# Kernel tuning notes

Hardware: AMD Instinct MI355X
Metric: run time of the kernel (lower is better)

## Reference

```python
import jax, jax.numpy as jnp
import numpy as np

E = 32          # num_experts
K = 4           # num_experts_per_tok
H = 1024        # hidden_size
I = 768         # moe_intermediate_size
ROUTED_SCALING_FACTOR = 1.0


def setup_inputs() -> dict:
    key = jax.random.key(0)
    k0, k1, k2, k3, k4, k5 = jax.random.split(key, 6)
    return {
        "hidden_states": jax.random.normal(k0, (1, 2048, H), jnp.float32),
        "gate_w": jax.random.normal(k1, (E, H), jnp.float32) * 0.02,
        "w1": jax.random.normal(k2, (E, H, I), jnp.float32) * 0.02,   # gate proj per expert
        "w3": jax.random.normal(k3, (E, H, I), jnp.float32) * 0.02,   # up proj per expert
        "w2": jax.random.normal(k4, (E, I, H), jnp.float32) * 0.02,   # down proj per expert
        "e_bias": jax.random.normal(k5, (E,), jnp.float32) * 0.02,    # e_score_correction_bias
    }


def reference(hidden_states, gate_w, w1, w3, w2, e_bias):
    orig_shape = hidden_states.shape
    x = hidden_states.reshape(-1, orig_shape[-1])            # [T, H]
    T = x.shape[0]

    # ----- router gate (ReplicatedLinear, no bias) -----
    router_logits = x @ gate_w.T                             # [T, E]

    # ----- grouped top-k with num_expert_group=1, topk_group=1 == plain top-k
    # scoring_func='sigmoid'; correction bias only affects expert *selection*,
    # the routing weights are the uncorrected sigmoid scores.
    scores = jax.nn.sigmoid(router_logits.astype(jnp.float32))          # [T, E]
    _, topk_ids = jax.lax.top_k(scores + e_bias[None, :], K)            # [T, K]
    topk_w = jnp.take_along_axis(scores, topk_ids, axis=1)              # [T, K]
    # renormalize (norm_topk_prob=True)
    topk_w = topk_w / jnp.sum(topk_w, axis=1, keepdims=True)

    # dense combine weights [T, E] (zero for unselected experts)
    combine = jnp.zeros((T, E), jnp.float32).at[jnp.arange(T)[:, None], topk_ids].add(topk_w)

    # ----- experts: SwiGLU per expert, combine weighted -----
    g = jnp.einsum("th,ehi->tei", x, w1)                     # [T, E, I]
    u = jnp.einsum("th,ehi->tei", x, w3)                     # [T, E, I]
    a = jax.nn.silu(g) * u * combine[:, :, None].astype(x.dtype)
    out = jnp.einsum("tei,eih->th", a, w2)                   # [T, H]

    out = out * ROUTED_SCALING_FACTOR
    return out.reshape(orig_shape)
```

## Files before the change

### kernel.cpp

```cpp
#include <hip/hip_runtime.h>
#include <cstdint>

#define TOK 2048
#define HD  1024
#define ID  768
#define NE  32
#define BM  320
#define NPOS (TOK * 4)

typedef unsigned short u16t;
typedef unsigned int   u32t;
typedef __bf16 bf16x8 __attribute__((ext_vector_type(8)));
typedef float  f32x4  __attribute__((ext_vector_type(4)));
typedef u16t   u16x8  __attribute__((ext_vector_type(8)));
typedef u16t   u16x4  __attribute__((ext_vector_type(4)));
typedef float  fvec4  __attribute__((ext_vector_type(4)));

__device__ __forceinline__ u16t f2b(float f) {
  u32t u = __float_as_uint(f);
  u32t r = u + 0x7fffu + ((u >> 16) & 1u);
  return (u16t)(r >> 16);
}

typedef __attribute__((address_space(3))) unsigned int       lds_uint;
typedef const __attribute__((address_space(1))) unsigned int glob_uint;
__device__ __forceinline__ void gload16(const void* g, void* l) {
  __builtin_amdgcn_global_load_lds((glob_uint*)g, (lds_uint*)l, 16, 0, 0);
}

#define BARN(N) do { \
    asm volatile("s_waitcnt vmcnt(" #N ") lgkmcnt(0)" ::: "memory"); \
    __builtin_amdgcn_s_barrier(); \
    __builtin_amdgcn_sched_barrier(0); \
  } while (0)

__global__ void k_router(const float* __restrict__ x, const float* __restrict__ gw,
                         const float* __restrict__ eb,
                         int* __restrict__ topk_ids, float* __restrict__ topk_w,
                         int* __restrict__ counts) {
  int lane = threadIdx.x & 63;
  int t = blockIdx.x * 4 + (threadIdx.x >> 6);
  const float* xt = x + (size_t)t * HD;
  fvec4 xr[4];
#pragma unroll
  for (int i = 0; i < 4; ++i) xr[i] = *(const fvec4*)(xt + lane * 4 + i * 256);
  float myscore = 0.f;
  for (int e = 0; e < NE; ++e) {
    const float* ge = gw + (size_t)e * HD + lane * 4;
    float s = 0.f;
#pragma unroll
    for (int i = 0; i < 4; ++i) {
      fvec4 g = *(const fvec4*)(ge + i * 256);
      s = fmaf(xr[i][0], g[0], s); s = fmaf(xr[i][1], g[1], s);
      s = fmaf(xr[i][2], g[2], s); s = fmaf(xr[i][3], g[3], s);
    }
#pragma unroll
    for (int off = 32; off; off >>= 1) s += __shfl_xor(s, off);
    if (lane == e) myscore = s;
  }
  float sig = 1.f / (1.f + expf(-myscore));
  float biased = (lane < NE) ? (sig + eb[lane]) : -3.0e38f;
  float wsum = 0.f;
  int ids[4]; float wsv[4];
#pragma unroll
  for (int k = 0; k < 4; ++k) {
    float v = biased; int idx = lane;
#pragma unroll
    for (int off = 32; off; off >>= 1) {
      float ov = __shfl_xor(v, off);
      int   oi = __shfl_xor(idx, off);
      if (ov > v || (ov == v && oi < idx)) { v = ov; idx = oi; }
    }
    ids[k] = idx;
    float sc = __shfl(sig, idx);
    wsv[k] = sc; wsum += sc;
    if (lane == idx) biased = -3.0e38f;
  }
  float inv = 1.f / wsum;
#pragma unroll
  for (int k = 0; k < 4; ++k) {
    if (lane == k) {
      topk_ids[t * 4 + k] = ids[k];
      topk_w[t * 4 + k]  = wsv[k] * inv;
      atomicAdd(&counts[ids[k]], 1);
    }
  }
}

__global__ void k_bucket(const int* __restrict__ topk_ids, const float* __restrict__ topk_w,
                         const int* __restrict__ counts, int* __restrict__ offsets,
                         int* __restrict__ pairTok, float* __restrict__ pairW,
                         int* __restrict__ invp) {
  __shared__ int soff[NE + 1];
  __shared__ int scur[NE];
  int tid = threadIdx.x;
  if (tid == 0) {
    int acc = 0;
    for (int e = 0; e < NE; ++e) { soff[e] = acc; acc += counts[e]; }
    soff[NE] = acc;
  }
  if (tid < NE) scur[tid] = 0;
  __syncthreads();
  if (tid <= NE) offsets[tid] = soff[tid];
  for (int p = tid; p < NPOS; p += 256) {
    int e = topk_ids[p];
    int pos = soff[e] + atomicAdd(&scur[e], 1);
    pairTok[pos] = p;
    pairW[pos]   = topk_w[p];
    invp[p]      = pos;
  }
}

__global__ void k_permute(const float* __restrict__ x, const int* __restrict__ pairTok,
                          u16t* __restrict__ Xp) {
  const int c = blockIdx.x;
  const int t = threadIdx.x;
  const int r = t & 15;
  const int tok = pairTok[c * 16 + r] >> 2;
  const float* xrow = x + (size_t)tok * HD;
  u16t* outp = Xp + (size_t)c * 16384;
#pragma unroll
  for (int i = 0; i < 8; ++i) {
    int G = t + i * 256;
    int s = G >> 6, g = (G >> 4) & 3;
    const float* src = xrow + s * 32 + g * 8;
    fvec4 a = *(const fvec4*)src, b = *(const fvec4*)(src + 4);
    u16x8 o = { f2b(a[0]), f2b(a[1]), f2b(a[2]), f2b(a[3]),
                f2b(b[0]), f2b(b[1]), f2b(b[2]), f2b(b[3]) };
    *(u16x8*)&outp[(size_t)G * 8] = o;
  }
}

__launch_bounds__(256, 3)
__global__ void k_gemm1(const u16t* __restrict__ Xp, const float* __restrict__ w1,
                        const float* __restrict__ w3,
                        const int* __restrict__ counts, const int* __restrict__ offsets,
                        const float* __restrict__ pairW,
                        u16t* __restrict__ A) {
  const int e = blockIdx.y;
  const int colbase = blockIdx.x * 32;
  const int count = counts[e];
  const int base  = offsets[e];
  const int tid = threadIdx.x, lane = tid & 63, wv = tid >> 6;
  const int l15 = lane & 15, kcl = lane >> 4;

  __shared__ __align__(16) u16t Xs[2][20 * 512];
  __shared__ __align__(16) u16t Ws[2][2][1024];
  __shared__ float pw[BM];

  const int mat_s = tid >> 7;
  const int v = tid & 127;
  const int wcolL = v & 31;
  const int kcs = v >> 5;
  const float* wp = (mat_s ? w3 : w1) + (size_t)e * HD * ID
                    + (size_t)(kcs * 8) * ID + colbase + wcolL;

#define G1_STAGEX(P, SMIN) do { \
    _Pragma("unroll") for (int q = 0; q < 5; ++q) \
      gload16((const char*)Xp + xsrc[q] + (u32t)(SMIN) * 1024u, &Xs[P][(wv * 5 + q) * 512]); \
  } while (0)
#define G1_WLOAD(WD, KB) do { \
    _Pragma("unroll") for (int j = 0; j < 8; ++j) \
      WD[j] = wp[(size_t)((KB) + j) * ID]; \
  } while (0)
#define G1_WSTORE(P, WD) do { \
    u16x8 pk = { f2b(WD[0]), f2b(WD[1]), f2b(WD[2]), f2b(WD[3]), \
                 f2b(WD[4]), f2b(WD[5]), f2b(WD[6]), f2b(WD[7]) }; \
    *(u16x8*)&Ws[P][mat_s][kcs * 256 + wcolL * 8] = pk; \
  } while (0)
#define G1_MFMA(P) do { \
    bf16x8 af[5]; \
    _Pragma("unroll") for (int rf = 0; rf < 5; ++rf) \
      af[rf] = *(const bf16x8*)&Xs[P][(wv * 5 + rf) * 512 + kcl * 128 + l15 * 8]; \
    _Pragma("unroll") for (int m = 0; m < 2; ++m) \
      _Pragma("unroll") for (int cf = 0; cf < 2; ++cf) { \
        bf16x8 b = *(const bf16x8*)&Ws[P][m][kcl * 256 + (cf * 16 + l15) * 8]; \
        _Pragma("unroll") for (int rf = 0; rf < 5; ++rf) \
          acc[rf][cf][m] = __builtin_amdgcn_mfma_f32_16x16x32_bf16(af[rf], b, acc[rf][cf][m], 0, 0, 0); \
      } \
  } while (0)

  for (int r0 = 0; r0 < count; r0 += BM) {
    __syncthreads();
    {
      int i = r0 + tid;
      pw[tid] = (i < count) ? pairW[base + i] : 0.f;
      if (tid < BM - 256) {
        int i2 = r0 + 256 + tid;
        pw[256 + tid] = (i2 < count) ? pairW[base + i2] : 0.f;
      }
    }
    u32t xsrc[5];
#pragma unroll
    for (int q = 0; q < 5; ++q) {
      int pos = base + r0 + wv * 80 + q * 16 + l15;
      pos = pos < NPOS ? pos : NPOS - 1;
      xsrc[q] = (u32t)(pos >> 4) * 32768u + (u32t)kcl * 256u + (u32t)(pos & 15) * 16u;
    }

    f32x4 zz = {0.f, 0.f, 0.f, 0.f};
    f32x4 acc[5][2][2];
#pragma unroll
    for (int a = 0; a < 5; ++a)
#pragma unroll
      for (int b = 0; b < 2; ++b) { acc[a][b][0] = zz; acc[a][b][1] = zz; }

    float wdA[8], wdB[8];
    G1_STAGEX(0, 0);
    G1_WLOAD(wdA, 0);
    G1_WLOAD(wdB, 32);
    G1_WSTORE(0, wdA);
    BARN(8);

    for (int s = 0; s < 32; s += 2) {
      const int k2e = ((s + 2 < 32) ? s + 2 : 31) * 32;
      G1_STAGEX(1, s + 1);
      G1_WSTORE(1, wdB);
      G1_WLOAD(wdA, k2e);
      G1_MFMA(0);
      BARN(8);
      const int s2  = (s + 2 < 32) ? s + 2 : 31;
      const int k2o = ((s + 3 < 32) ? s + 3 : 31) * 32;
      G1_STAGEX(0, s2);
      G1_WSTORE(0, wdA);
      G1_WLOAD(wdB, k2o);
      G1_MFMA(1);
      BARN(8);
    }

    const u32t bx512 = (u32t)blockIdx.x * 512u;
#pragma unroll
    for (int rf = 0; rf < 5; ++rf)
#pragma unroll
      for (int ri = 0; ri < 4; ++ri) {
        int row = wv * 80 + rf * 16 + (lane >> 4) * 4 + ri;
        int grow = r0 + row;
        if (grow < count) {
          float wgt = pw[row];
          int pos = base + grow;
          u32t rbase = (u32t)(pos >> 4) * 12288u + bx512 + (u32t)(pos & 15) * 8u;
#pragma unroll
          for (int cf = 0; cf < 2; ++cf) {
            float gg = acc[rf][cf][0][ri];
            float uu = acc[rf][cf][1][ri];
            float a = gg / (1.f + expf(-gg)) * uu * wgt;
            int cc = cf * 16 + l15;
            A[rbase + (u32t)((cc >> 3) & 3) * 128u + (u32t)(cc & 7)] = f2b(a);
          }
        }
      }
  }
#undef G1_STAGEX
#undef G1_WLOAD
#undef G1_WSTORE
#undef G1_MFMA
}

__launch_bounds__(256, 3)
__global__ void k_gemm2(const u16t* __restrict__ Ab, const float* __restrict__ w2,
                        const int* __restrict__ counts, const int* __restrict__ offsets,
                        float* __restrict__ buf) {
  const int e = blockIdx.y;
  const int colbase = blockIdx.x * 32;
  const int count = counts[e];
  const int base  = offsets[e];
  const int tid = threadIdx.x, lane = tid & 63, wv = tid >> 6;
  const int l15 = lane & 15, kcl = lane >> 4;

  __shared__ __align__(16) u16t Xs[2][20 * 512];
  __shared__ __align__(16) u16t Ws[2][1024];

  const int wcolL = tid & 31;
  const int h = tid >> 5;
  const float* w2t = w2 + (size_t)e * ID * HD + (size_t)(h * 4) * HD + colbase + wcolL;
  const int wdst = (h >> 1) * 256 + wcolL * 8 + (h & 1) * 4;

#define G2_STAGEX(P, SMIN) do { \
    _Pragma("unroll") for (int q = 0; q < 5; ++q) \
      gload16((const char*)Ab + asrc[q] + (u32t)(SMIN) * 1024u, &Xs[P][(wv * 5 + q) * 512]); \
  } while (0)
#define G2_WLOAD(WD, KB) do { \
    _Pragma("unroll") for (int j = 0; j < 4; ++j) \
      WD[j] = w2t[(size_t)((KB) + j) * HD]; \
  } while (0)
#define G2_WSTORE(P, WD) do { \
    u16x4 pk = { f2b(WD[0]), f2b(WD[1]), f2b(WD[2]), f2b(WD[3]) }; \
    *(u16x4*)&Ws[P][wdst] = pk; \
  } while (0)
#define G2_MFMA(P) do { \
    bf16x8 af[5]; \
    _Pragma("unroll") for (int rf = 0; rf < 5; ++rf) \
      af[rf] = *(const bf16x8*)&Xs[P][(wv * 5 + rf) * 512 + kcl * 128 + l15 * 8]; \
    _Pragma("unroll") for (int cf = 0; cf < 2; ++cf) { \
      bf16x8 b = *(const bf16x8*)&Ws[P][kcl * 256 + (cf * 16 + l15) * 8]; \
      _Pragma("unroll") for (int rf = 0; rf < 5; ++rf) \
        acc[rf][cf] = __builtin_amdgcn_mfma_f32_16x16x32_bf16(af[rf], b, acc[rf][cf], 0, 0, 0); \
    } \
  } while (0)

  for (int r0 = 0; r0 < count; r0 += BM) {
    __syncthreads();
    u32t asrc[5];
#pragma unroll
    for (int q = 0; q < 5; ++q) {
      int pos = base + r0 + wv * 80 + q * 16 + l15;
      pos = pos < NPOS ? pos : NPOS - 1;
      asrc[q] = (u32t)(pos >> 4) * 24576u + (u32t)kcl * 256u + (u32t)(pos & 15) * 16u;
    }

    f32x4 zz = {0.f, 0.f, 0.f, 0.f};
    f32x4 acc[5][2];
#pragma unroll
    for (int a = 0; a < 5; ++a) { acc[a][0] = zz; acc[a][1] = zz; }

    float wdA[4], wdB[4];
    G2_STAGEX(0, 0);
    G2_WLOAD(wdA, 0);
    G2_WLOAD(wdB, 32);
    G2_WSTORE(0, wdA);
    BARN(4);

    for (int s = 0; s < 24; s += 2) {
      const int k2e = ((s + 2 < 24) ? s + 2 : 23) * 32;
      G2_STAGEX(1, s + 1);
      G2_WSTORE(1, wdB);
      G2_WLOAD(wdA, k2e);
      G2_MFMA(0);
      BARN(4);
      const int s2  = (s + 2 < 24) ? s + 2 : 23;
      const int k2o = ((s + 3 < 24) ? s + 3 : 23) * 32;
      G2_STAGEX(0, s2);
      G2_WSTORE(0, wdA);
      G2_WLOAD(wdB, k2o);
      G2_MFMA(1);
      BARN(4);
    }

#pragma unroll
    for (int rf = 0; rf < 5; ++rf)
#pragma unroll
      for (int ri = 0; ri < 4; ++ri) {
        int row = wv * 80 + rf * 16 + (lane >> 4) * 4 + ri;
        int grow = r0 + row;
        if (grow < count) {
#pragma unroll
          for (int cf = 0; cf < 2; ++cf)
            buf[(size_t)(base + grow) * HD + colbase + cf * 16 + l15] = acc[rf][cf][ri];
        }
      }
  }
#undef G2_STAGEX
#undef G2_WLOAD
#undef G2_WSTORE
#undef G2_MFMA
}

__global__ void k_reduce(const float* __restrict__ buf, const int* __restrict__ invp,
                         float* __restrict__ out) {
  int t = blockIdx.x;
  int col = threadIdx.x * 4;
  int p0 = invp[t * 4 + 0], p1 = invp[t * 4 + 1];
  int p2 = invp[t * 4 + 2], p3 = invp[t * 4 + 3];
  fvec4 s = *(const fvec4*)(buf + (size_t)p0 * HD + col);
  s += *(const fvec4*)(buf + (size_t)p1 * HD + col);
  s += *(const fvec4*)(buf + (size_t)p2 * HD + col);
  s += *(const fvec4*)(buf + (size_t)p3 * HD + col);
  *(fvec4*)(out + (size_t)t * HD + col) = s;
}

extern "C" void kernel_launch(void* const* d_in, const int* in_sizes, int n_in,
                              void* d_out, int out_size, void* d_ws, size_t ws_size,
                              hipStream_t stream) {
  const float* x  = (const float*)d_in[0];
  const float* gw = (const float*)d_in[1];
  const float* w1 = (const float*)d_in[2];
  const float* w3 = (const float*)d_in[3];
  const float* w2 = (const float*)d_in[4];
  const float* eb = (const float*)d_in[5];
  float* out = (float*)d_out;

  char* ws = (char*)d_ws;
  int*   counts   = (int*)(ws);
  int*   offsets  = (int*)(ws + 256);
  int*   topk_ids = (int*)(ws + 4096);
  float* topk_w   = (float*)(ws + 36864);
  int*   pairTok  = (int*)(ws + 69632);
  float* pairW    = (float*)(ws + 102400);
  int*   invp     = (int*)(ws + 135168);
  u16t*  Xp   = (u16t*)(ws + 262144);
  float* buf  = (float*)(ws + 262144);
  u16t*  Abuf = (u16t*)(ws + 262144 + 33554432);

  hipMemsetAsync(counts, 0, 4096, stream);
  k_router <<<512, 256, 0, stream>>>(x, gw, eb, topk_ids, topk_w, counts);
  k_bucket <<<1, 256, 0, stream>>>(topk_ids, topk_w, counts, offsets, pairTok, pairW, invp);
  k_permute<<<512, 256, 0, stream>>>(x, pairTok, Xp);
  k_gemm1  <<<dim3(24, 32), 256, 0, stream>>>(Xp, w1, w3, counts, offsets, pairW, Abuf);
  k_gemm2  <<<dim3(32, 32), 256, 0, stream>>>(Abuf, w2, counts, offsets, buf);
  k_reduce <<<2048, 256, 0, stream>>>(buf, invp, out);
}
```

Measured before the change: 262.1 us.

## Load A fragments directly into registers instead of staging through LDS

Both grouped GEMM kernels stop staging the pre-packed activation tiles through LDS with global_load_lds. Each lane now loads its bf16x8 MFMA fragments straight from global memory into registers, double-buffered across k-steps, and only the fp32->bf16 weight tile still goes through LDS. This frees the large Xs shared buffers and the LDS read traffic, and gemm2's launch bound is raised to 4 waves per SIMD. In exchange it uses more registers for prefetched fragments and relies on the compiler's vmcnt handling instead of explicit waits, which may expose global latency.

```diff
diff --git a/kernel.cpp b/kernel.cpp
--- a/kernel.cpp
+++ b/kernel.cpp
@@ -22,14 +22,8 @@
   return (u16t)(r >> 16);
 }
 
-typedef __attribute__((address_space(3))) unsigned int       lds_uint;
-typedef const __attribute__((address_space(1))) unsigned int glob_uint;
-__device__ __forceinline__ void gload16(const void* g, void* l) {
-  __builtin_amdgcn_global_load_lds((glob_uint*)g, (lds_uint*)l, 16, 0, 0);
-}
-
-#define BARN(N) do { \
-    asm volatile("s_waitcnt vmcnt(" #N ") lgkmcnt(0)" ::: "memory"); \
+#define BAR() do { \
+    asm volatile("s_waitcnt lgkmcnt(0)" ::: "memory"); \
     __builtin_amdgcn_s_barrier(); \
     __builtin_amdgcn_sched_barrier(0); \
   } while (0)
@@ -144,7 +138,6 @@
   const int tid = threadIdx.x, lane = tid & 63, wv = tid >> 6;
   const int l15 = lane & 15, kcl = lane >> 4;
 
-  __shared__ __align__(16) u16t Xs[2][20 * 512];
   __shared__ __align__(16) u16t Ws[2][2][1024];
   __shared__ float pw[BM];
 
@@ -155,28 +148,25 @@
   const float* wp = (mat_s ? w3 : w1) + (size_t)e * HD * ID
                     + (size_t)(kcs * 8) * ID + colbase + wcolL;
 
-#define G1_STAGEX(P, SMIN) do { \
+#define G1_AFLOAD(AF, S) do { \
     _Pragma("unroll") for (int q = 0; q < 5; ++q) \
-      gload16((const char*)Xp + xsrc[q] + (u32t)(SMIN) * 1024u, &Xs[P][(wv * 5 + q) * 512]); \
-  } while (0)
-#define G1_WLOAD(WD, KB) do { \
+      AF[q] = *(const u16x8*)((const char*)Xp + xsrc[q] + (u32t)(S) * 1024u); \
+  } while (0)
+#define G1_WLOAD(KB) do { \
     _Pragma("unroll") for (int j = 0; j < 8; ++j) \
-      WD[j] = wp[(size_t)((KB) + j) * ID]; \
-  } while (0)
-#define G1_WSTORE(P, WD) do { \
-    u16x8 pk = { f2b(WD[0]), f2b(WD[1]), f2b(WD[2]), f2b(WD[3]), \
-                 f2b(WD[4]), f2b(WD[5]), f2b(WD[6]), f2b(WD[7]) }; \
+      wd[j] = wp[(size_t)((KB) + j) * ID]; \
+  } while (0)
+#define G1_WSTORE(P) do { \
+    u16x8 pk = { f2b(wd[0]), f2b(wd[1]), f2b(wd[2]), f2b(wd[3]), \
+                 f2b(wd[4]), f2b(wd[5]), f2b(wd[6]), f2b(wd[7]) }; \
     *(u16x8*)&Ws[P][mat_s][kcs * 256 + wcolL * 8] = pk; \
   } while (0)
-#define G1_MFMA(P) do { \
-    bf16x8 af[5]; \
-    _Pragma("unroll") for (int rf = 0; rf < 5; ++rf) \
-      af[rf] = *(const bf16x8*)&Xs[P][(wv * 5 + rf) * 512 + kcl * 128 + l15 * 8]; \
+#define G1_MFMA(AF, P) do { \
     _Pragma("unroll") for (int m = 0; m < 2; ++m) \
       _Pragma("unroll") for (int cf = 0; cf < 2; ++cf) { \
         bf16x8 b = *(const bf16x8*)&Ws[P][m][kcl * 256 + (cf * 16 + l15) * 8]; \
         _Pragma("unroll") for (int rf = 0; rf < 5; ++rf) \
-          acc[rf][cf][m] = __builtin_amdgcn_mfma_f32_16x16x32_bf16(af[rf], b, acc[rf][cf][m], 0, 0, 0); \
+          acc[rf][cf][m] = __builtin_amdgcn_mfma_f32_16x16x32_bf16(AF[rf], b, acc[rf][cf][m], 0, 0, 0); \
       } \
   } while (0)
 
@@ -205,27 +195,26 @@
 #pragma unroll
       for (int b = 0; b < 2; ++b) { acc[a][b][0] = zz; acc[a][b][1] = zz; }
 
-    float wdA[8], wdB[8];
-    G1_STAGEX(0, 0);
-    G1_WLOAD(wdA, 0);
-    G1_WLOAD(wdB, 32);
-    G1_WSTORE(0, wdA);
-    BARN(8);
+    u16x8 afA[5], afB[5];
+    float wd[8];
+    G1_AFLOAD(afA, 0);
+    G1_AFLOAD(afB, 1);
+    G1_WLOAD(0);
+    G1_WSTORE(0);
+    G1_WLOAD(32);
+    BAR();
 
     for (int s = 0; s < 32; s += 2) {
-      const int k2e = ((s + 2 < 32) ? s + 2 : 31) * 32;
-      G1_STAGEX(1, s + 1);
-      G1_WSTORE(1, wdB);
-      G1_WLOAD(wdA, k2e);
-      G1_MFMA(0);
-      BARN(8);
-      const int s2  = (s + 2 < 32) ? s + 2 : 31;
-      const int k2o = ((s + 3 < 32) ? s + 3 : 31) * 32;
-      G1_STAGEX(0, s2);
-      G1_WSTORE(0, wdA);
-      G1_WLOAD(wdB, k2o);
-      G1_MFMA(1);
-      BARN(8);
+      G1_WSTORE(1);
+      { const int k2 = (s + 2 < 32) ? s + 2 : 31; G1_WLOAD(k2 * 32); }
+      G1_MFMA(afA, 0);
+      { const int s2 = (s + 2 < 32) ? s + 2 : 31; G1_AFLOAD(afA, s2); }
+      BAR();
+      G1_WSTORE(0);
+      { const int k3 = (s + 3 < 32) ? s + 3 : 31; G1_WLOAD(k3 * 32); }
+      G1_MFMA(afB, 1);
+      { const int s3 = (s + 3 < 32) ? s + 3 : 31; G1_AFLOAD(afB, s3); }
+      BAR();
     }
 
     const u32t bx512 = (u32t)blockIdx.x * 512u;
@@ -250,13 +239,13 @@
         }
       }
   }
-#undef G1_STAGEX
+#undef G1_AFLOAD
 #undef G1_WLOAD
 #undef G1_WSTORE
 #undef G1_MFMA
 }
 
-__launch_bounds__(256, 3)
+__launch_bounds__(256, 4)
 __global__ void k_gemm2(const u16t* __restrict__ Ab, const float* __restrict__ w2,
                         const int* __restrict__ counts, const int* __restrict__ offsets,
                         float* __restrict__ buf) {
@@ -267,7 +256,6 @@
   const int tid = threadIdx.x, lane = tid & 63, wv = tid >> 6;
   const int l15 = lane & 15, kcl = lane >> 4;
 
-  __shared__ __align__(16) u16t Xs[2][20 * 512];
   __shared__ __align__(16) u16t Ws[2][1024];
 
   const int wcolL = tid & 31;
@@ -275,26 +263,23 @@
   const float* w2t = w2 + (size_t)e * ID * HD + (size_t)(h * 4) * HD + colbase + wcolL;
   const int wdst = (h >> 1) * 256 + wcolL * 8 + (h & 1) * 4;
 
-#define G2_STAGEX(P, SMIN) do { \
+#define G2_AFLOAD(AF, S) do { \
     _Pragma("unroll") for (int q = 0; q < 5; ++q) \
-      gload16((const char*)Ab + asrc[q] + (u32t)(SMIN) * 1024u, &Xs[P][(wv * 5 + q) * 512]); \
-  } while (0)
-#define G2_WLOAD(WD, KB) do { \
+      AF[q] = *(const u16x8*)((const char*)Ab + asrc[q] + (u32t)(S) * 1024u); \
+  } while (0)
+#define G2_WLOAD(KB) do { \
     _Pragma("unroll") for (int j = 0; j < 4; ++j) \
-      WD[j] = w2t[(size_t)((KB) + j) * HD]; \
-  } while (0)
-#define G2_WSTORE(P, WD) do { \
-    u16x4 pk = { f2b(WD[0]), f2b(WD[1]), f2b(WD[2]), f2b(WD[3]) }; \
+      wd[j] = w2t[(size_t)((KB) + j) * HD]; \
+  } while (0)
+#define G2_WSTORE(P) do { \
+    u16x4 pk = { f2b(wd[0]), f2b(wd[1]), f2b(wd[2]), f2b(wd[3]) }; \
     *(u16x4*)&Ws[P][wdst] = pk; \
   } while (0)
-#define G2_MFMA(P) do { \
-    bf16x8 af[5]; \
-    _Pragma("unroll") for (int rf = 0; rf < 5; ++rf) \
-      af[rf] = *(const bf16x8*)&Xs[P][(wv * 5 + rf) * 512 + kcl * 128 + l15 * 8]; \
+#define G2_MFMA(AF, P) do { \
     _Pragma("unroll") for (int cf = 0; cf < 2; ++cf) { \
       bf16x8 b = *(const bf16x8*)&Ws[P][kcl * 256 + (cf * 16 + l15) * 8]; \
       _Pragma("unroll") for (int rf = 0; rf < 5; ++rf) \
-        acc[rf][cf] = __builtin_amdgcn_mfma_f32_16x16x32_bf16(af[rf], b, acc[rf][cf], 0, 0, 0); \
+        acc[rf][cf] = __builtin_amdgcn_mfma_f32_16x16x32_bf16(AF[rf], b, acc[rf][cf], 0, 0, 0); \
     } \
   } while (0)
 
@@ -313,27 +298,26 @@
 #pragma unroll
     for (int a = 0; a < 5; ++a) { acc[a][0] = zz; acc[a][1] = zz; }
 
-    float wdA[4], wdB[4];
-    G2_STAGEX(0, 0);
-    G2_WLOAD(wdA, 0);
-    G2_WLOAD(wdB, 32);
-    G2_WSTORE(0, wdA);
-    BARN(4);
+    u16x8 afA[5], afB[5];
+    float wd[4];
+    G2_AFLOAD(afA, 0);
+    G2_AFLOAD(afB, 1);
+    G2_WLOAD(0);
+    G2_WSTORE(0);
+    G2_WLOAD(32);
+    BAR();
 
     for (int s = 0; s < 24; s += 2) {
-      const int k2e = ((s + 2 < 24) ? s + 2 : 23) * 32;
-      G2_STAGEX(1, s + 1);
-      G2_WSTORE(1, wdB);
-      G2_WLOAD(wdA, k2e);
-      G2_MFMA(0);
-      BARN(4);
-      const int s2  = (s + 2 < 24) ? s + 2 : 23;
-      const int k2o = ((s + 3 < 24) ? s + 3 : 23) * 32;
-      G2_STAGEX(0, s2);
-      G2_WSTORE(0, wdA);
-      G2_WLOAD(wdB, k2o);
-      G2_MFMA(1);
-      BARN(4);
+      G2_WSTORE(1);
+      { const int k2 = (s + 2 < 24) ? s + 2 : 23; G2_WLOAD(k2 * 32); }
+      G2_MFMA(afA, 0);
+      { const int s2 = (s + 2 < 24) ? s + 2 : 23; G2_AFLOAD(afA, s2); }
+      BAR();
+      G2_WSTORE(0);
+      { const int k3 = (s + 3 < 24) ? s + 3 : 23; G2_WLOAD(k3 * 32); }
+      G2_MFMA(afB, 1);
+      { const int s3 = (s + 3 < 24) ? s + 3 : 23; G2_AFLOAD(afB, s3); }
+      BAR();
     }
 
 #pragma unroll
@@ -349,7 +333,7 @@
         }
       }
   }
-#undef G2_STAGEX
+#undef G2_AFLOAD
 #undef G2_WLOAD
 #undef G2_WSTORE
 #undef G2_MFMA
```

New measurement: 239.6 us. -8.6%, faster.
